# Performance work log

Hardware: AMD Instinct MI355X
Metric: run time of the kernel (lower is better)

## Reference

```python
import jax, jax.numpy as jnp
import numpy as np


def setup_inputs() -> dict:
    key = jax.random.key(0)
    k1, k2 = jax.random.split(key)
    B, C, H, W = 4, 128, 192, 640
    left = jax.random.normal(k1, (B, C, H, W), dtype=jnp.float32)
    right = jax.random.normal(k2, (B, C, H, W), dtype=jnp.float32)
    return {"left": left, "right": right, "num_disparities": 96}


def reference(left, right, num_disparities):
    """Dot-product stereo cost volume (is_right=False).

    cost[b, d, y, x] = sum_c left[b, c, y, x] * right[b, c, y, x - d],
    with zeros where x - d < 0.  Output: [B, D, H, W].
    """
    D = num_disparities
    B, C, H, W = left.shape
    # Zero-pad right on the left edge of the width axis so that the slice
    # starting at (D-1-d) gives right shifted by d with zero fill.
    right_pad = jnp.pad(right, ((0, 0), (0, 0), (0, 0), (D - 1, 0)))

    def per_disparity(d):
        r = jax.lax.dynamic_slice_in_dim(right_pad, (D - 1) - d, W, axis=3)
        return jnp.sum(left * r, axis=1)  # [B, H, W], reduce over channels

    cost = jax.lax.map(per_disparity, jnp.arange(D))  # [D, B, H, W]
    return jnp.transpose(cost, (1, 0, 2, 3))  # [B, D, H, W]
```

## Files before the change

kernel.cpp:

```cpp
#include <hip/hip_runtime.h>

#define Bn 4
#define Cn 128
#define Hn 192
#define Wn 640
#define Dn 96
#define HW (Hn * Wn)

#define PR 184
#define PL 88
#define EP 68

typedef float f32x4 __attribute__((ext_vector_type(4)));
typedef short short8 __attribute__((ext_vector_type(8)));

__device__ __forceinline__ unsigned short f2bf(float f) {
  unsigned int u = __builtin_bit_cast(unsigned int, f);
  u += 0x7FFFu + ((u >> 16) & 1u);
  return (unsigned short)(u >> 16);
}

union SMem {
  struct {
    unsigned short R[32 * PR];
    unsigned short L[32 * PL];
  } s;
  float epi[48 * EP];
};

__global__ __launch_bounds__(256, 6) void cost_volume_kernel(
    const float* __restrict__ left, const float* __restrict__ right,
    float* __restrict__ out) {
  __shared__ SMem sm;

  const int x0 = blockIdx.x * 64;
  const int y  = blockIdx.y;
  const int b  = blockIdx.z;
  const int t  = threadIdx.x;
  const int w  = t >> 6;
  const int n  = t & 15;
  const int q  = (t >> 4) & 3;

  f32x4 acc[7];
#pragma unroll
  for (int jj = 0; jj < 7; ++jj) acc[jj] = (f32x4){0.f, 0.f, 0.f, 0.f};

  const int tc  = t >> 3;
  const int tv  = t & 7;
  const int swz = (tc >> 3) & 3;
  const float* lrow = left  + ((size_t)(b * Cn) * Hn + y) * Wn + x0;
  const float* rrow = right + ((size_t)(b * Cn) * Hn + y) * Wn + x0 - 96;

  ushort4 hv[7];
  auto load_chunk = [&](int ck) {
    const size_t coff = (size_t)(ck + tc) * HW;
#pragma unroll
    for (int i = 0; i < 5; ++i) {
      const int ue = 4 * tv + 32 * i;
      f32x4 v = (f32x4){0.f, 0.f, 0.f, 0.f};
      if (x0 + ue >= 96) v = *(const f32x4*)(rrow + coff + ue);
      hv[i].x = f2bf(v.x); hv[i].y = f2bf(v.y); hv[i].z = f2bf(v.z); hv[i].w = f2bf(v.w);
    }
#pragma unroll
    for (int i = 0; i < 2; ++i) {
      const int ue = 4 * tv + 32 * i;
      f32x4 v = *(const f32x4*)(lrow + coff + ue);
      hv[5 + i].x = f2bf(v.x); hv[5 + i].y = f2bf(v.y);
      hv[5 + i].z = f2bf(v.z); hv[5 + i].w = f2bf(v.w);
    }
  };

  load_chunk(0);
#pragma unroll
  for (int kk = 0; kk < 4; ++kk) {
    __syncthreads();
#pragma unroll
    for (int i = 0; i < 5; ++i) {
      const int ue = 4 * tv + 32 * i;
      *(ushort4*)&sm.s.R[tc * PR + ue + 8 * swz] = hv[i];
    }
#pragma unroll
    for (int i = 0; i < 2; ++i) {
      const int ue = 4 * tv + 32 * i;
      *(ushort4*)&sm.s.L[tc * PL + ue + 8 * swz] = hv[5 + i];
    }
    __syncthreads();
    if (kk < 3) load_chunk(32 * (kk + 1));

    {
      const unsigned short* Lp = &sm.s.L[(8 * q) * PL + 16 * w + n + 8 * q];
      short8 bf;
#pragma unroll
      for (int j = 0; j < 8; ++j) bf[j] = (short)Lp[j * PL];
      const unsigned short* Rp = &sm.s.R[(8 * q) * PR + 16 * w + n + 8 * q];
#pragma unroll
      for (int jj = 0; jj < 7; ++jj) {
        short8 af;
#pragma unroll
        for (int j = 0; j < 8; ++j) af[j] = (short)Rp[j * PR + 16 * jj];
        acc[jj] = __builtin_amdgcn_mfma_f32_16x16x32_bf16(af, bf, acc[jj], 0, 0, 0);
      }
    }
  }

#pragma unroll
  for (int p = 0; p < 2; ++p) {
    __syncthreads();
#pragma unroll
    for (int jj = 0; jj < 7; ++jj)
#pragma unroll
      for (int r = 0; r < 4; ++r) {
        const int d = 96 + n - 16 * jj - 4 * q - r - 48 * p;
        if (d >= 0 && d < 48) sm.epi[d * EP + 16 * w + n] = acc[jj][r];
      }
    __syncthreads();
    const size_t obase = (((size_t)b * Dn + 48 * p) * Hn + y) * Wn + x0;
    const int tx = (t & 15) << 2;
    const int d0 = t >> 4;
#pragma unroll
    for (int ii = 0; ii < 3; ++ii) {
      const int d = d0 + 16 * ii;
      f32x4 v = *(const f32x4*)&sm.epi[d * EP + tx];
      *(f32x4*)&out[obase + (size_t)d * HW + tx] = v;
    }
  }
}

extern "C" void kernel_launch(void* const* d_in, const int* in_sizes, int n_in,
                              void* d_out, int out_size, void* d_ws, size_t ws_size,
                              hipStream_t stream) {
  const float* left  = (const float*)d_in[0];
  const float* right = (const float*)d_in[1];
  float* out = (float*)d_out;
  dim3 grid(Wn / 64, Hn, Bn);
  cost_volume_kernel<<<grid, dim3(256, 1, 1), 0, stream>>>(left, right, out);
}
```

Before: 553.6 us.

## Transpose shared-memory tiles to channel-contiguous layout for vectorized MFMA operand loads

Changes the LDS layout of the bf16 left/right tiles from channel-major (pixel-contiguous) to pixel-major with channels contiguous. Each MFMA operand then comes from one 16-byte LDS read instead of eight scalar 2-byte reads. To fill this layout, global loads become scalar per-channel loads (8 channels per thread, coalesced across lanes), each packed into a 16-byte LDS write. In exchange, global loads lose float4 vectorization, register use rises, and launch bounds drop from 6 to 5 blocks per SM.

```diff
diff --git a/kernel.cpp b/kernel.cpp
--- a/kernel.cpp
+++ b/kernel.cpp
@@ -7,12 +7,13 @@
 #define Dn 96
 #define HW (Hn * Wn)
 
-#define PR 184
-#define PL 88
+#define PRh 40
+#define PLh 40
 #define EP 68
 
 typedef float f32x4 __attribute__((ext_vector_type(4)));
 typedef short short8 __attribute__((ext_vector_type(8)));
+typedef unsigned short ushort8 __attribute__((ext_vector_type(8)));
 
 __device__ __forceinline__ unsigned short f2bf(float f) {
   unsigned int u = __builtin_bit_cast(unsigned int, f);
@@ -22,13 +23,13 @@
 
 union SMem {
   struct {
-    unsigned short R[32 * PR];
-    unsigned short L[32 * PL];
+    unsigned short R[160 * PRh];
+    unsigned short L[64 * PLh];
   } s;
   float epi[48 * EP];
 };
 
-__global__ __launch_bounds__(256, 6) void cost_volume_kernel(
+__global__ __launch_bounds__(256, 5) void cost_volume_kernel(
     const float* __restrict__ left, const float* __restrict__ right,
     float* __restrict__ out) {
   __shared__ SMem sm;
@@ -38,6 +39,7 @@
   const int b  = blockIdx.z;
   const int t  = threadIdx.x;
   const int w  = t >> 6;
+  const int l  = t & 63;
   const int n  = t & 15;
   const int q  = (t >> 4) & 3;
 
@@ -45,29 +47,23 @@
 #pragma unroll
   for (int jj = 0; jj < 7; ++jj) acc[jj] = (f32x4){0.f, 0.f, 0.f, 0.f};
 
-  const int tc  = t >> 3;
-  const int tv  = t & 7;
-  const int swz = (tc >> 3) & 3;
   const float* lrow = left  + ((size_t)(b * Cn) * Hn + y) * Wn + x0;
   const float* rrow = right + ((size_t)(b * Cn) * Hn + y) * Wn + x0 - 96;
 
-  ushort4 hv[7];
+  float rv[3][8];
+  float lv[8];
   auto load_chunk = [&](int ck) {
-    const size_t coff = (size_t)(ck + tc) * HW;
+    const float* rb = rrow + (size_t)(ck + 8 * w) * HW;
 #pragma unroll
-    for (int i = 0; i < 5; ++i) {
-      const int ue = 4 * tv + 32 * i;
-      f32x4 v = (f32x4){0.f, 0.f, 0.f, 0.f};
-      if (x0 + ue >= 96) v = *(const f32x4*)(rrow + coff + ue);
-      hv[i].x = f2bf(v.x); hv[i].y = f2bf(v.y); hv[i].z = f2bf(v.z); hv[i].w = f2bf(v.w);
+    for (int i = 0; i < 3; ++i) {
+      const int u = l + 64 * i;
+      const bool ok = (u < 160) && (x0 + u >= 96);
+#pragma unroll
+      for (int j = 0; j < 8; ++j) rv[i][j] = ok ? rb[(size_t)j * HW + u] : 0.f;
     }
+    const float* lb = lrow + (size_t)(ck + 8 * w) * HW;
 #pragma unroll
-    for (int i = 0; i < 2; ++i) {
-      const int ue = 4 * tv + 32 * i;
-      f32x4 v = *(const f32x4*)(lrow + coff + ue);
-      hv[5 + i].x = f2bf(v.x); hv[5 + i].y = f2bf(v.y);
-      hv[5 + i].z = f2bf(v.z); hv[5 + i].w = f2bf(v.w);
-    }
+    for (int j = 0; j < 8; ++j) lv[j] = lb[(size_t)j * HW + l];
   };
 
   load_chunk(0);
@@ -75,29 +71,30 @@
   for (int kk = 0; kk < 4; ++kk) {
     __syncthreads();
 #pragma unroll
-    for (int i = 0; i < 5; ++i) {
-      const int ue = 4 * tv + 32 * i;
-      *(ushort4*)&sm.s.R[tc * PR + ue + 8 * swz] = hv[i];
+    for (int i = 0; i < 3; ++i) {
+      const int u = l + 64 * i;
+      if (u < 160) {
+        ushort8 pk;
+#pragma unroll
+        for (int j = 0; j < 8; ++j) pk[j] = f2bf(rv[i][j]);
+        *(ushort8*)&sm.s.R[u * PRh + 8 * w] = pk;
+      }
     }
+    {
+      ushort8 pl;
 #pragma unroll
-    for (int i = 0; i < 2; ++i) {
-      const int ue = 4 * tv + 32 * i;
-      *(ushort4*)&sm.s.L[tc * PL + ue + 8 * swz] = hv[5 + i];
+      for (int j = 0; j < 8; ++j) pl[j] = f2bf(lv[j]);
+      *(ushort8*)&sm.s.L[l * PLh + 8 * w] = pl;
     }
     __syncthreads();
     if (kk < 3) load_chunk(32 * (kk + 1));
 
     {
-      const unsigned short* Lp = &sm.s.L[(8 * q) * PL + 16 * w + n + 8 * q];
-      short8 bf;
-#pragma unroll
-      for (int j = 0; j < 8; ++j) bf[j] = (short)Lp[j * PL];
-      const unsigned short* Rp = &sm.s.R[(8 * q) * PR + 16 * w + n + 8 * q];
+      const short8 bf = *(const short8*)&sm.s.L[(16 * w + n) * PLh + 8 * q];
 #pragma unroll
       for (int jj = 0; jj < 7; ++jj) {
-        short8 af;
-#pragma unroll
-        for (int j = 0; j < 8; ++j) af[j] = (short)Rp[j * PR + 16 * jj];
+        const short8 af =
+            *(const short8*)&sm.s.R[(16 * w + 16 * jj + n) * PRh + 8 * q];
         acc[jj] = __builtin_amdgcn_mfma_f32_16x16x32_bf16(af, bf, acc[jj], 0, 0, 0);
       }
     }
```

Result: no change. 554.2 us (+0.1%).
